# Optimization experiments

Measured on AMD Instinct MI355X. Metric: run time of the kernel, lower is better.

Reference implementation:

```python
import jax, jax.numpy as jnp
import numpy as np

T, B, F, H = 1024, 64, 256, 512


def setup_inputs() -> dict:
    key = jax.random.key(0)
    k0, k1, k2 = jax.random.split(key, 3)
    s_i = 1.0 / np.sqrt(F)  # lecun_normal-ish scaling for input kernels
    s_h = 1.0 / np.sqrt(H)  # orthogonal-ish scaling for recurrent kernels
    return {
        "x": jax.random.normal(k0, (T, B, F), jnp.float32),
        "h0": jnp.zeros((B, H), jnp.float32),  # flax initialize_carry -> zeros
        "Wi": jax.random.normal(k1, (F, 3 * H), jnp.float32) * s_i,   # [ir|iz|in]
        "bi": jnp.zeros((3 * H,), jnp.float32),
        "Wh": jax.random.normal(k2, (H, 3 * H), jnp.float32) * s_h,   # [hr|hz|hn]
        "bhn": jnp.zeros((H,), jnp.float32),  # only the 'n' hidden dense has bias
    }


def reference(x, h0, Wi, bi, Wh, bhn):
    # Precompute all input-to-hidden projections in one big GEMM (math-equivalent
    # to doing them per step inside the scan, but far more efficient).
    xg = jnp.einsum('tbf,fg->tbg', x, Wi) + bi  # (T, B, 3H)

    def step(h, xg_t):
        hg = h @ Wh                              # (B, 3H)
        xr, xz, xn = jnp.split(xg_t, 3, axis=-1)
        hr, hz, hn = jnp.split(hg, 3, axis=-1)
        r = jax.nn.sigmoid(xr + hr)
        z = jax.nn.sigmoid(xz + hz)
        n = jnp.tanh(xn + r * (hn + bhn))
        h_new = (1.0 - z) * n + z * h            # flax GRUCell update
        return h_new, h_new

    _, ys = jax.lax.scan(step, h0, xg)
    return ys  # (T, B, H); final carry == ys[-1]
```

## Files before the change

kernel.cpp:

```cpp
#include <hip/hip_runtime.h>
#include <stdint.h>

#define NB 32

typedef __attribute__((ext_vector_type(8))) short short8;
typedef __attribute__((ext_vector_type(4))) float floatx4;

__device__ __forceinline__ unsigned short f2bf(float f) {
  unsigned u = __float_as_uint(f);
  u += 0x7fff + ((u >> 16) & 1);
  return (unsigned short)(u >> 16);
}
__device__ __forceinline__ float bf2f(unsigned short s) {
  return __uint_as_float(((unsigned)s) << 16);
}

__global__ __launch_bounds__(256) void prep_kernel(
    const float* __restrict__ x, const float* __restrict__ h0,
    const float* __restrict__ Wi, const float* __restrict__ Wh,
    unsigned short* __restrict__ xbf, unsigned short* __restrict__ wit,
    unsigned short* __restrict__ wht, unsigned short* __restrict__ hbf,
    unsigned int* __restrict__ ctr) {
  int i = blockIdx.x * 256 + threadIdx.x;
  if (i < 4194304) {
    float4 v = ((const float4*)x)[i];
    ushort4 o;
    o.x = f2bf(v.x); o.y = f2bf(v.y); o.z = f2bf(v.z); o.w = f2bf(v.w);
    ((ushort4*)xbf)[i] = o;
  } else if (i < 4587520) {
    int j = i - 4194304;
    int n = j >> 8, k = j & 255;
    wit[j] = f2bf(Wi[(size_t)k * 1536 + n]);
  } else if (i < 5373952) {
    int j = i - 4587520;
    int n = j >> 9, k = j & 511;
    wht[j] = f2bf(Wh[(size_t)k * 1536 + n]);
  } else if (i < 5406720) {
    int j = i - 5373952;
    hbf[j] = f2bf(h0[j]);
  } else if (i == 5406720) {
    *ctr = 0u;
  }
}

__global__ __launch_bounds__(256, 2) void gemm_xg(
    const unsigned short* __restrict__ A,
    const unsigned short* __restrict__ BT,
    const float* __restrict__ bi,
    unsigned short* __restrict__ C) {
  __shared__ __align__(16) unsigned short lA[128 * 72];
  __shared__ __align__(16) unsigned short lB[128 * 72];
  const int tid = threadIdx.x;
  const int w = tid >> 6, lane = tid & 63;
  const int wm = w >> 1, wn = w & 1;
  const int q = lane >> 4, l16 = lane & 15;
  const int bx = blockIdx.x, by = blockIdx.y;

  floatx4 acc[4][4];
#pragma unroll
  for (int a = 0; a < 4; ++a)
#pragma unroll
    for (int b = 0; b < 4; ++b) acc[a][b] = (floatx4){0.f, 0.f, 0.f, 0.f};

  for (int kt = 0; kt < 4; ++kt) {
    if (kt) __syncthreads();
#pragma unroll
    for (int i = 0; i < 4; ++i) {
      int c = tid + i * 256;
      int r = c >> 3, kk = (c & 7) * 8;
      *(uint4*)&lA[r * 72 + kk] =
          *(const uint4*)&A[(size_t)(bx * 128 + r) * 256 + kt * 64 + kk];
      *(uint4*)&lB[r * 72 + kk] =
          *(const uint4*)&BT[(size_t)(by * 128 + r) * 256 + kt * 64 + kk];
    }
    __syncthreads();
#pragma unroll
    for (int ks = 0; ks < 2; ++ks) {
      const int kk = ks * 32 + q * 8;
      short8 af[4], bf[4];
#pragma unroll
      for (int rm = 0; rm < 4; ++rm)
        af[rm] = *(const short8*)&lA[(wm * 64 + rm * 16 + l16) * 72 + kk];
#pragma unroll
      for (int cn = 0; cn < 4; ++cn)
        bf[cn] = *(const short8*)&lB[(wn * 64 + cn * 16 + l16) * 72 + kk];
#pragma unroll
      for (int rm = 0; rm < 4; ++rm)
#pragma unroll
        for (int cn = 0; cn < 4; ++cn)
          acc[rm][cn] = __builtin_amdgcn_mfma_f32_16x16x32_bf16(
              af[rm], bf[cn], acc[rm][cn], 0, 0, 0);
    }
  }
#pragma unroll
  for (int cn = 0; cn < 4; ++cn) {
    const int col = by * 128 + wn * 64 + cn * 16 + l16;
    const float bic = bi[col];
#pragma unroll
    for (int rm = 0; rm < 4; ++rm)
#pragma unroll
      for (int r = 0; r < 4; ++r) {
        const int row = bx * 128 + wm * 64 + rm * 16 + q * 4 + r;
        C[(size_t)row * 1536 + col] = f2bf(acc[rm][cn][r] + bic);
      }
  }
}

__global__ __launch_bounds__(256, 1) void scan_kernel(
    const unsigned short* __restrict__ xg,
    const unsigned short* __restrict__ wht,
    const float* __restrict__ h0, const float* __restrict__ bhn,
    float* __restrict__ ys,
    unsigned short* __restrict__ hbf,
    unsigned int* __restrict__ ctr) {
  const int tid = threadIdx.x;
  const int w = tid >> 6, lane = tid & 63;
  const int q = lane >> 4, l16 = lane & 15;
  const int i0 = blockIdx.x * 16;

  short8 bfr[3][16];
#pragma unroll
  for (int g = 0; g < 3; ++g)
#pragma unroll
    for (int s = 0; s < 16; ++s)
      bfr[g][s] = *(const short8*)
          &wht[(size_t)(g * 512 + i0 + l16) * 512 + s * 32 + q * 8];

  const int dim = i0 + l16;
  const float bhn_c = bhn[dim];
  const int bc0 = w * 16 + q * 4;
  const int ba = w * 16 + l16;

  float hreg[4];
#pragma unroll
  for (int r = 0; r < 4; ++r) hreg[r] = h0[(size_t)(bc0 + r) * 512 + dim];

  float xgv[3][4];
#pragma unroll
  for (int r = 0; r < 4; ++r) {
    size_t xb = (size_t)(bc0 + r) * 1536 + dim;
    xgv[0][r] = bf2f(xg[xb]);
    xgv[1][r] = bf2f(xg[xb + 512]);
    xgv[2][r] = bf2f(xg[xb + 1024]);
  }

  for (int t = 0; t < 1024; ++t) {
    const unsigned short* hsrc = hbf + (size_t)(t & 1) * 32768;
    unsigned short* hdst = hbf + (size_t)((t + 1) & 1) * 32768;

    short8 af[16];
#pragma unroll
    for (int s = 0; s < 16; ++s)
      af[s] = *(const short8*)&hsrc[(size_t)ba * 512 + s * 32 + q * 8];

    floatx4 a0 = {0.f, 0.f, 0.f, 0.f};
    floatx4 a1 = {0.f, 0.f, 0.f, 0.f};
    floatx4 a2 = {0.f, 0.f, 0.f, 0.f};
#pragma unroll
    for (int s = 0; s < 16; ++s) {
      a0 = __builtin_amdgcn_mfma_f32_16x16x32_bf16(af[s], bfr[0][s], a0, 0, 0, 0);
      a1 = __builtin_amdgcn_mfma_f32_16x16x32_bf16(af[s], bfr[1][s], a1, 0, 0, 0);
      a2 = __builtin_amdgcn_mfma_f32_16x16x32_bf16(af[s], bfr[2][s], a2, 0, 0, 0);
    }

#pragma unroll
    for (int r = 0; r < 4; ++r) {
      const int bc = bc0 + r;
      float rg = 1.f / (1.f + __expf(-(xgv[0][r] + a0[r])));
      float zg = 1.f / (1.f + __expf(-(xgv[1][r] + a1[r])));
      float pre = xgv[2][r] + rg * (a2[r] + bhn_c);
      pre = fminf(fmaxf(pre, -15.f), 15.f);
      float e2 = __expf(2.f * pre);
      float ng = (e2 - 1.f) / (e2 + 1.f);
      float hnew = (1.f - zg) * ng + zg * hreg[r];
      hreg[r] = hnew;
      ys[((size_t)t * 64 + bc) * 512 + dim] = hnew;
      hdst[(size_t)bc * 512 + dim] = f2bf(hnew);
    }

    if (t != 1023) {
#pragma unroll
      for (int r = 0; r < 4; ++r) {
        size_t xb = ((size_t)(t + 1) * 64 + bc0 + r) * 1536 + dim;
        xgv[0][r] = bf2f(xg[xb]);
        xgv[1][r] = bf2f(xg[xb + 512]);
        xgv[2][r] = bf2f(xg[xb + 1024]);
      }
      __syncthreads();
      if (tid == 0) {
        __threadfence();
        atomicAdd(ctr, 1u);
        const unsigned tgt = (unsigned)NB * (unsigned)(t + 1);
        while (__hip_atomic_load(ctr, __ATOMIC_RELAXED,
                                 __HIP_MEMORY_SCOPE_AGENT) < tgt) {}
        __threadfence();
      }
      __syncthreads();
    }
  }
}

extern "C" void kernel_launch(void* const* d_in, const int* in_sizes, int n_in,
                              void* d_out, int out_size, void* d_ws, size_t ws_size,
                              hipStream_t stream) {
  const float* x   = (const float*)d_in[0];
  const float* h0  = (const float*)d_in[1];
  const float* Wi  = (const float*)d_in[2];
  const float* bi  = (const float*)d_in[3];
  const float* Wh  = (const float*)d_in[4];
  const float* bhn = (const float*)d_in[5];
  float* ys = (float*)d_out;

  char* ws = (char*)d_ws;
  unsigned short* xg  = (unsigned short*)(ws);
  unsigned short* xbf = (unsigned short*)(ws + 201326592);
  unsigned short* wit = (unsigned short*)(ws + 234881024);
  unsigned short* wht = (unsigned short*)(ws + 235667456);
  unsigned short* hbf = (unsigned short*)(ws + 237240320);
  unsigned int*   ctr = (unsigned int*)(ws + 237371392);

  prep_kernel<<<21121, 256, 0, stream>>>(x, h0, Wi, Wh, xbf, wit, wht, hbf, ctr);
  gemm_xg<<<dim3(512, 12), 256, 0, stream>>>(xbf, wit, bi, xg);
  scan_kernel<<<NB, 256, 0, stream>>>(xg, wht, h0, bhn, ys, hbf, ctr);
}
```

Before: 7.288 ms.

## Replace global counter barrier with per-element step-tagged hidden-state flags

Drops the per-step grid-wide atomic counter barrier and __syncthreads pair. Each hidden-state element is now stored as a 32-bit word holding a step tag in the high half and the bf16 value in the low half. Consumers spin on their own 8-element slices until every tag matches the current step, which gives fine-grained dataflow synchronisation. The cost is double the hidden-state traffic, a poll-and-reload loop per MFMA slice, and reliance on relaxed atomics for ordering of the tagged words. The xg prefetch for the next step is also moved to the current step.

```diff
diff --git a/kernel.cpp b/kernel.cpp
--- a/kernel.cpp
+++ b/kernel.cpp
@@ -15,12 +15,16 @@
   return __uint_as_float(((unsigned)s) << 16);
 }
 
+__device__ __forceinline__ unsigned long long ald64(const unsigned* p) {
+  return __hip_atomic_load((const unsigned long long*)p,
+                           __ATOMIC_RELAXED, __HIP_MEMORY_SCOPE_AGENT);
+}
+
 __global__ __launch_bounds__(256) void prep_kernel(
     const float* __restrict__ x, const float* __restrict__ h0,
     const float* __restrict__ Wi, const float* __restrict__ Wh,
     unsigned short* __restrict__ xbf, unsigned short* __restrict__ wit,
-    unsigned short* __restrict__ wht, unsigned short* __restrict__ hbf,
-    unsigned int* __restrict__ ctr) {
+    unsigned short* __restrict__ wht, unsigned* __restrict__ hsf) {
   int i = blockIdx.x * 256 + threadIdx.x;
   if (i < 4194304) {
     float4 v = ((const float4*)x)[i];
@@ -37,9 +41,12 @@
     wht[j] = f2bf(Wh[(size_t)k * 1536 + n]);
   } else if (i < 5406720) {
     int j = i - 5373952;
-    hbf[j] = f2bf(h0[j]);
-  } else if (i == 5406720) {
-    *ctr = 0u;
+    __hip_atomic_store(&hsf[j], (unsigned)f2bf(h0[j]),
+                       __ATOMIC_RELAXED, __HIP_MEMORY_SCOPE_AGENT);
+  } else if (i < 5439488) {
+    int j = i - 5406720;
+    __hip_atomic_store(&hsf[32768 + j], 0xFFFF0000u,
+                       __ATOMIC_RELAXED, __HIP_MEMORY_SCOPE_AGENT);
   }
 }
 
@@ -111,8 +118,7 @@
     const unsigned short* __restrict__ wht,
     const float* __restrict__ h0, const float* __restrict__ bhn,
     float* __restrict__ ys,
-    unsigned short* __restrict__ hbf,
-    unsigned int* __restrict__ ctr) {
+    unsigned* __restrict__ hsf) {
   const int tid = threadIdx.x;
   const int w = tid >> 6, lane = tid & 63;
   const int q = lane >> 4, l16 = lane & 15;
@@ -135,67 +141,69 @@
 #pragma unroll
   for (int r = 0; r < 4; ++r) hreg[r] = h0[(size_t)(bc0 + r) * 512 + dim];
 
-  float xgv[3][4];
-#pragma unroll
-  for (int r = 0; r < 4; ++r) {
-    size_t xb = (size_t)(bc0 + r) * 1536 + dim;
-    xgv[0][r] = bf2f(xg[xb]);
-    xgv[1][r] = bf2f(xg[xb + 512]);
-    xgv[2][r] = bf2f(xg[xb + 1024]);
-  }
-
   for (int t = 0; t < 1024; ++t) {
-    const unsigned short* hsrc = hbf + (size_t)(t & 1) * 32768;
-    unsigned short* hdst = hbf + (size_t)((t + 1) & 1) * 32768;
-
-    short8 af[16];
-#pragma unroll
-    for (int s = 0; s < 16; ++s)
-      af[s] = *(const short8*)&hsrc[(size_t)ba * 512 + s * 32 + q * 8];
-
+    const unsigned* src = hsf + (size_t)(t & 1) * 32768;
+    unsigned* dst = hsf + (size_t)((t + 1) & 1) * 32768;
+
+    unsigned long long st[16][4];
+#pragma unroll
+    for (int s = 0; s < 16; ++s) {
+      const unsigned* p = src + ba * 512 + s * 32 + q * 8;
+#pragma unroll
+      for (int j = 0; j < 4; ++j) st[s][j] = ald64(p + j * 2);
+    }
+    float xcur[3][4];
+#pragma unroll
+    for (int r = 0; r < 4; ++r) {
+      size_t xb = ((size_t)t * 64 + bc0 + r) * 1536 + dim;
+      xcur[0][r] = bf2f(xg[xb]);
+      xcur[1][r] = bf2f(xg[xb + 512]);
+      xcur[2][r] = bf2f(xg[xb + 1024]);
+    }
+
+    const unsigned e = ((unsigned)t) << 16;
     floatx4 a0 = {0.f, 0.f, 0.f, 0.f};
     floatx4 a1 = {0.f, 0.f, 0.f, 0.f};
     floatx4 a2 = {0.f, 0.f, 0.f, 0.f};
 #pragma unroll
     for (int s = 0; s < 16; ++s) {
-      a0 = __builtin_amdgcn_mfma_f32_16x16x32_bf16(af[s], bfr[0][s], a0, 0, 0, 0);
-      a1 = __builtin_amdgcn_mfma_f32_16x16x32_bf16(af[s], bfr[1][s], a1, 0, 0, 0);
-      a2 = __builtin_amdgcn_mfma_f32_16x16x32_bf16(af[s], bfr[2][s], a2, 0, 0, 0);
-    }
-
+      unsigned long long v0 = st[s][0], v1 = st[s][1];
+      unsigned long long v2 = st[s][2], v3 = st[s][3];
+      for (;;) {
+        unsigned m = ((unsigned)v0 ^ e) | ((unsigned)(v0 >> 32) ^ e) |
+                     ((unsigned)v1 ^ e) | ((unsigned)(v1 >> 32) ^ e) |
+                     ((unsigned)v2 ^ e) | ((unsigned)(v2 >> 32) ^ e) |
+                     ((unsigned)v3 ^ e) | ((unsigned)(v3 >> 32) ^ e);
+        if (__ballot((m & 0xffff0000u) == 0u) == ~0ull) break;
+        const unsigned* p = src + ba * 512 + s * 32 + q * 8;
+        v0 = ald64(p); v1 = ald64(p + 2); v2 = ald64(p + 4); v3 = ald64(p + 6);
+      }
+      union { unsigned u[4]; short8 s8; } pk;
+      pk.u[0] = ((unsigned)v0 & 0xffffu) | ((unsigned)(v0 >> 32) << 16);
+      pk.u[1] = ((unsigned)v1 & 0xffffu) | ((unsigned)(v1 >> 32) << 16);
+      pk.u[2] = ((unsigned)v2 & 0xffffu) | ((unsigned)(v2 >> 32) << 16);
+      pk.u[3] = ((unsigned)v3 & 0xffffu) | ((unsigned)(v3 >> 32) << 16);
+      a0 = __builtin_amdgcn_mfma_f32_16x16x32_bf16(pk.s8, bfr[0][s], a0, 0, 0, 0);
+      a1 = __builtin_amdgcn_mfma_f32_16x16x32_bf16(pk.s8, bfr[1][s], a1, 0, 0, 0);
+      a2 = __builtin_amdgcn_mfma_f32_16x16x32_bf16(pk.s8, bfr[2][s], a2, 0, 0, 0);
+    }
+
+    const unsigned ns = ((unsigned)(t + 1)) << 16;
 #pragma unroll
     for (int r = 0; r < 4; ++r) {
       const int bc = bc0 + r;
-      float rg = 1.f / (1.f + __expf(-(xgv[0][r] + a0[r])));
-      float zg = 1.f / (1.f + __expf(-(xgv[1][r] + a1[r])));
-      float pre = xgv[2][r] + rg * (a2[r] + bhn_c);
+      float rg = 1.f / (1.f + __expf(-(xcur[0][r] + a0[r])));
+      float zg = 1.f / (1.f + __expf(-(xcur[1][r] + a1[r])));
+      float pre = xcur[2][r] + rg * (a2[r] + bhn_c);
       pre = fminf(fmaxf(pre, -15.f), 15.f);
       float e2 = __expf(2.f * pre);
       float ng = (e2 - 1.f) / (e2 + 1.f);
       float hnew = (1.f - zg) * ng + zg * hreg[r];
       hreg[r] = hnew;
+      if (t != 1023)
+        __hip_atomic_store(&dst[(size_t)bc * 512 + dim], ns | f2bf(hnew),
+                           __ATOMIC_RELAXED, __HIP_MEMORY_SCOPE_AGENT);
       ys[((size_t)t * 64 + bc) * 512 + dim] = hnew;
-      hdst[(size_t)bc * 512 + dim] = f2bf(hnew);
-    }
-
-    if (t != 1023) {
-#pragma unroll
-      for (int r = 0; r < 4; ++r) {
-        size_t xb = ((size_t)(t + 1) * 64 + bc0 + r) * 1536 + dim;
-        xgv[0][r] = bf2f(xg[xb]);
-        xgv[1][r] = bf2f(xg[xb + 512]);
-        xgv[2][r] = bf2f(xg[xb + 1024]);
-      }
-      __syncthreads();
-      if (tid == 0) {
-        __threadfence();
-        atomicAdd(ctr, 1u);
-        const unsigned tgt = (unsigned)NB * (unsigned)(t + 1);
-        while (__hip_atomic_load(ctr, __ATOMIC_RELAXED,
-                                 __HIP_MEMORY_SCOPE_AGENT) < tgt) {}
-        __threadfence();
-      }
-      __syncthreads();
     }
   }
 }
@@ -216,10 +224,9 @@
   unsigned short* xbf = (unsigned short*)(ws + 201326592);
   unsigned short* wit = (unsigned short*)(ws + 234881024);
   unsigned short* wht = (unsigned short*)(ws + 235667456);
-  unsigned short* hbf = (unsigned short*)(ws + 237240320);
-  unsigned int*   ctr = (unsigned int*)(ws + 237371392);
-
-  prep_kernel<<<21121, 256, 0, stream>>>(x, h0, Wi, Wh, xbf, wit, wht, hbf, ctr);
+  unsigned*       hsf = (unsigned*)(ws + 237240320);
+
+  prep_kernel<<<21248, 256, 0, stream>>>(x, h0, Wi, Wh, xbf, wit, wht, hsf);
   gemm_xg<<<dim3(512, 12), 256, 0, stream>>>(xbf, wit, bi, xg);
-  scan_kernel<<<NB, 256, 0, stream>>>(xg, wht, h0, bhn, ys, hbf, ctr);
-}
+  scan_kernel<<<NB, 256, 0, stream>>>(xg, wht, h0, bhn, ys, hsf);
+}
```

After: 16.60 ms. 128% more time.
